# Optimization experiments

Hardware: AMD Instinct MI355X
Metric: run time of the kernel (lower is better)

## Reference

```python
import jax, jax.numpy as jnp
import numpy as np

B, S, D, H = 2, 2048, 1024, 16
HD = D // H


def setup_inputs() -> dict:
    key = jax.random.key(0)
    ks = jax.random.split(key, 12)
    s = 1.0 / np.sqrt(D)
    inp = {
        "queries": jax.random.normal(ks[0], (B, S, D), jnp.float32),
        "keys": jax.random.normal(ks[1], (B, S, D), jnp.float32),
        "values": jax.random.normal(ks[2], (B, S, D), jnp.float32),
        # True = masked out (causal upper triangle)
        "attn_mask": jnp.triu(jnp.ones((S, S), bool), k=1),
        "W_q": jax.random.normal(ks[3], (D, D), jnp.float32) * s,
        "b_q": jnp.zeros((D,), jnp.float32),
        "W_k": jax.random.normal(ks[4], (D, D), jnp.float32) * s,
        "b_k": jnp.zeros((D,), jnp.float32),
        "W_v": jax.random.normal(ks[5], (D, D), jnp.float32) * s,
        "b_v": jnp.zeros((D,), jnp.float32),
        "W_o": jax.random.normal(ks[6], (D, D), jnp.float32) * s,
        "b_o": jnp.zeros((D,), jnp.float32),
    }
    return inp


def _split_heads(x):
    b, s, _ = x.shape
    return x.reshape(b, s, H, HD).transpose(0, 2, 1, 3)  # (B,H,S,HD)


def reference(queries, keys, values, attn_mask, W_q, b_q, W_k, b_k, W_v, b_v, W_o, b_o):
    Q = _split_heads(queries @ W_q + b_q)
    K = _split_heads(keys @ W_k + b_k)
    V = _split_heads(values @ W_v + b_v)
    scale = 1.0 / np.sqrt(HD)
    scores = jnp.einsum("bhqd,bhkd->bhqk", Q, K) * scale  # (B,H,S,S)
    scores = jnp.where(attn_mask, jnp.float32(-1e9), scores)
    probs = jax.nn.softmax(scores, axis=-1)
    ctx = jnp.einsum("bhqk,bhkd->bhqd", probs, V)
    ctx = ctx.transpose(0, 2, 1, 3).reshape(queries.shape[0], queries.shape[1], D)
    return ctx @ W_o + b_o
```

## Files before the change

kernel.cpp:

```cpp
#include <hip/hip_runtime.h>
#include <hip/hip_bf16.h>
#include <math.h>

typedef __bf16 bf16x8 __attribute__((ext_vector_type(8)));
typedef float f32x4 __attribute__((ext_vector_type(4)));
typedef unsigned short u16x8 __attribute__((ext_vector_type(8)));
typedef unsigned short u16x4 __attribute__((ext_vector_type(4)));

static __device__ __forceinline__ unsigned short f2bf(float f) {
    union { float f; unsigned u; } v; v.f = f;
    unsigned r = v.u + 0x7fffu + ((v.u >> 16) & 1u);
    return (unsigned short)(r >> 16);
}

static __device__ __forceinline__ float exp2fast(float x) {
    return __builtin_exp2f(x);
}

static __device__ __forceinline__ void gload16(const void* g, void* l) {
    __builtin_amdgcn_global_load_lds((const __attribute__((address_space(1))) unsigned int*)g,
                                     (__attribute__((address_space(3))) unsigned int*)l, 16, 0, 0);
}

#define MFMA16(a, b, c) __builtin_amdgcn_mfma_f32_16x16x32_bf16((a), (b), (c), 0, 0, 0)

static __device__ __forceinline__ bf16x8 frag_swz(const unsigned short* base, int row, int chunk) {
    return *(const bf16x8*)((const char*)base + row * 128 + (((chunk ^ row) & 7) << 4));
}

__global__ void conv_bf16_kernel(const float* __restrict__ in, unsigned short* __restrict__ out) {
    const size_t i = ((size_t)blockIdx.x * 256 + threadIdx.x) * 8;
    f32x4 v0 = *(const f32x4*)(in + i);
    f32x4 v1 = *(const f32x4*)(in + i + 4);
    u16x8 o;
#pragma unroll
    for (int j = 0; j < 4; ++j) { o[j] = f2bf(v0[j]); o[j + 4] = f2bf(v1[j]); }
    *(u16x8*)(out + i) = o;
}

__global__ void conv_wt_kernel(const float* __restrict__ W, unsigned short* __restrict__ Wt) {
    __shared__ __align__(16) unsigned short Ws[64][66];
    const int t = threadIdx.x;
    const int r0 = blockIdx.y * 64;
    const int c0 = blockIdx.x * 64;
#pragma unroll
    for (int p = 0; p < 4; ++p) {
        int lin = p * 256 + t;
        int r = lin >> 4, cc = (lin & 15) * 4;
        f32x4 v = *(const f32x4*)(W + (size_t)(r0 + r) * 1024 + c0 + cc);
#pragma unroll
        for (int j = 0; j < 4; ++j) Ws[r][cc + j] = f2bf(v[j]);
    }
    __syncthreads();
#pragma unroll
    for (int p = 0; p < 2; ++p) {
        int lin = p * 256 + t;
        int n = lin >> 3, kc = (lin & 7) * 8;
        u16x8 o;
#pragma unroll
        for (int j = 0; j < 8; ++j) o[j] = Ws[kc + j][n];
        *(u16x8*)(Wt + (size_t)(c0 + n) * 1024 + r0 + kc) = o;
    }
}

template<int OMODE>
__global__ __launch_bounds__(256, 2)
void gemm_bt(const unsigned short* __restrict__ A, const unsigned short* __restrict__ Bt,
             const float* __restrict__ bias, void* __restrict__ Outp,
             int M, int N, int K, float oscale)
{
    __shared__ __align__(16) unsigned short As[2][128 * 64];
    __shared__ __align__(16) unsigned short Bs[2][128 * 64];

    const int t = threadIdx.x, lane = t & 63, w = t >> 6;
    const int lr = lane & 15, lh = lane >> 4;
    const int m0 = blockIdx.y * 128, n0 = blockIdx.x * 128;
    const int wm = (w >> 1) * 64, wn = (w & 1) * 64;
    const int nkt = K >> 6;
    const int wbase = (t & 0xC0) * 8;

    f32x4 acc[4][4];
#pragma unroll
    for (int i = 0; i < 4; ++i)
#pragma unroll
        for (int j = 0; j < 4; ++j)
#pragma unroll
            for (int e = 0; e < 4; ++e) acc[i][j][e] = 0.0f;

    auto stage = [&](int buf, int kt) {
        const int k0 = kt << 6;
#pragma unroll
        for (int q = 0; q < 4; ++q) {
            int lin = q * 256 + t;
            int row = lin >> 3, sc = (lin ^ (lin >> 3)) & 7;
            gload16(A + (size_t)(m0 + row) * K + k0 + sc * 8, &As[buf][q * 2048 + wbase]);
        }
#pragma unroll
        for (int q = 0; q < 4; ++q) {
            int lin = q * 256 + t;
            int row = lin >> 3, sc = (lin ^ (lin >> 3)) & 7;
            gload16(Bt + (size_t)(n0 + row) * K + k0 + sc * 8, &Bs[buf][q * 2048 + wbase]);
        }
    };

    stage(0, 0);
    for (int kt = 0; kt < nkt; ++kt) {
        __syncthreads();
        if (kt + 1 < nkt) stage((kt + 1) & 1, kt + 1);
        const unsigned short* as = As[kt & 1];
        const unsigned short* bs = Bs[kt & 1];
#pragma unroll
        for (int kb = 0; kb < 2; ++kb) {
            bf16x8 a[4], b[4];
#pragma unroll
            for (int i = 0; i < 4; ++i) a[i] = frag_swz(as, wm + i * 16 + lr, kb * 4 + lh);
#pragma unroll
            for (int j = 0; j < 4; ++j) b[j] = frag_swz(bs, wn + j * 16 + lr, kb * 4 + lh);
#pragma unroll
            for (int i = 0; i < 4; ++i)
#pragma unroll
                for (int j = 0; j < 4; ++j)
                    acc[i][j] = MFMA16(a[i], b[j], acc[i][j]);
        }
    }

#pragma unroll
    for (int i = 0; i < 4; ++i) {
#pragma unroll
        for (int j = 0; j < 4; ++j) {
            const int gcol = n0 + wn + j * 16 + lr;
            const float bv = bias[gcol];
            if (OMODE == 0) {
#pragma unroll
                for (int r = 0; r < 4; ++r) {
                    const int grow = m0 + wm + i * 16 + lh * 4 + r;
                    ((float*)Outp)[(size_t)grow * N + gcol] = (acc[i][j][r] + bv) * oscale;
                }
            } else if (OMODE == 1) {
#pragma unroll
                for (int r = 0; r < 4; ++r) {
                    const int grow = m0 + wm + i * 16 + lh * 4 + r;
                    const int b_ = grow >> 11, s_ = grow & 2047;
                    const int h_ = gcol >> 6, hd_ = gcol & 63;
                    ((unsigned short*)Outp)[((size_t)((b_ * 16 + h_) * 2048 + s_) << 6) + hd_] =
                        f2bf((acc[i][j][r] + bv) * oscale);
                }
            } else {
                const int grow0 = m0 + wm + i * 16 + lh * 4;
                const int b_ = grow0 >> 11, s_ = grow0 & 2047;
                const int h_ = gcol >> 6, hd_ = gcol & 63;
                u16x4 pk;
#pragma unroll
                for (int r = 0; r < 4; ++r) pk[r] = f2bf((acc[i][j][r] + bv) * oscale);
                *(u16x4*)((unsigned short*)Outp + (((size_t)((b_ * 16 + h_) * 64 + hd_)) << 11) + s_) = pk;
            }
        }
    }
}

__global__ __launch_bounds__(256, 2)
void attn_kernel(const unsigned short* __restrict__ Qp,
                 const unsigned short* __restrict__ Kp,
                 const unsigned short* __restrict__ Vtp,
                 unsigned short* __restrict__ Cp)
{
    __shared__ __align__(16) unsigned short Ks[2][64 * 64];
    __shared__ __align__(16) unsigned short Vs[2][64 * 64];
    __shared__ __align__(16) unsigned short Pl[4][16 * 64];

    const int t = threadIdx.x, lane = t & 63, w = t >> 6;
    const int lr = lane & 15, lh = lane >> 4;
    const int wbase = (t & 0xC0) * 8;

    const int g = blockIdx.x;
    const int local = g >> 3;
    const int bh = (g & 7) * 4 + (local >> 4);
    const int qA = local & 15;
    const size_t baseQK = (size_t)bh * (2048 * 64);
    const size_t baseV  = (size_t)bh * (64 * 2048);

    auto stageKV = [&](int buf, int kv0) {
#pragma unroll
        for (int q = 0; q < 2; ++q) {
            int lin = q * 256 + t;
            int row = lin >> 3, sc = (lin ^ (lin >> 3)) & 7;
            gload16(Kp + baseQK + (size_t)(kv0 + row) * 64 + sc * 8, &Ks[buf][q * 2048 + wbase]);
        }
#pragma unroll
        for (int q = 0; q < 2; ++q) {
            int lin = q * 256 + t;
            int row = lin >> 3, sc = (lin ^ (lin >> 3)) & 7;
            gload16(Vtp + baseV + (size_t)row * 2048 + kv0 + sc * 8, &Vs[buf][q * 2048 + wbase]);
        }
    };

    unsigned short* pl = &Pl[w][0];
    const int b_ = bh >> 4, h_ = bh & 15;

    for (int qi = 0; qi < 2; ++qi) {
        const int qt = qi ? (31 - qA) : qA;
        const int q0w = qt * 64 + w * 16;
        const int ntiles = qt + 1;

        const unsigned short* qrow = Qp + baseQK + (size_t)(q0w + lr) * 64 + lh * 8;
        const bf16x8 qf0 = *(const bf16x8*)qrow;
        const bf16x8 qf1 = *(const bf16x8*)(qrow + 32);

        f32x4 o[4]; float m[4], l[4];
#pragma unroll
        for (int i = 0; i < 4; ++i) {
#pragma unroll
            for (int e = 0; e < 4; ++e) o[i][e] = 0.0f;
            m[i] = -INFINITY; l[i] = 0.0f;
        }

        __syncthreads();
        stageKV(0, 0);
        for (int tt = 0; tt < ntiles; ++tt) {
            __syncthreads();
            if (tt + 1 < ntiles) stageKV((tt + 1) & 1, (tt + 1) * 64);
            const unsigned short* ks = Ks[tt & 1];
            const unsigned short* vs = Vs[tt & 1];

            f32x4 s[4];
#pragma unroll
            for (int c = 0; c < 4; ++c) {
#pragma unroll
                for (int e = 0; e < 4; ++e) s[c][e] = 0.0f;
                s[c] = MFMA16(qf0, frag_swz(ks, c * 16 + lr, lh), s[c]);
                s[c] = MFMA16(qf1, frag_swz(ks, c * 16 + lr, 4 + lh), s[c]);
            }

            const bool diag = (tt == qt);
            const int kv0 = tt * 64;
#pragma unroll
            for (int r = 0; r < 4; ++r) {
                const int row = lh * 4 + r;
                const int grow = q0w + row;
                float tv[4];
#pragma unroll
                for (int c = 0; c < 4; ++c) {
                    float x = s[c][r];
                    if (diag && (kv0 + c * 16 + lr > grow)) x = -1e30f;
                    tv[c] = x;
                }
                float cm = fmaxf(fmaxf(tv[0], tv[1]), fmaxf(tv[2], tv[3]));
                cm = fmaxf(cm, __shfl_xor(cm, 1));
                cm = fmaxf(cm, __shfl_xor(cm, 2));
                cm = fmaxf(cm, __shfl_xor(cm, 4));
                cm = fmaxf(cm, __shfl_xor(cm, 8));
                if (!__all(cm <= m[r] + 11.0f)) {
                    const float mn = fmaxf(m[r], cm);
                    const float al = exp2fast(m[r] - mn);
#pragma unroll
                    for (int hc = 0; hc < 4; ++hc) o[hc][r] *= al;
                    l[r] *= al;
                    m[r] = mn;
                }
                float rs = 0.0f;
#pragma unroll
                for (int c = 0; c < 4; ++c) {
                    const float p = exp2fast(tv[c] - m[r]);
                    rs += p;
                    *(unsigned short*)((char*)pl + row * 128 +
                        ((c * 32 + lr * 2) ^ ((row & 7) << 4))) = f2bf(p);
                }
                l[r] += rs;
            }

            const bf16x8 pf0 = frag_swz(pl, lr, lh);
            const bf16x8 pf1 = frag_swz(pl, lr, 4 + lh);
#pragma unroll
            for (int hc = 0; hc < 4; ++hc) {
                o[hc] = MFMA16(pf0, frag_swz(vs, hc * 16 + lr, lh), o[hc]);
                o[hc] = MFMA16(pf1, frag_swz(vs, hc * 16 + lr, 4 + lh), o[hc]);
            }
        }

#pragma unroll
        for (int r = 0; r < 4; ++r) {
            float sum = l[r];
            sum += __shfl_xor(sum, 1);
            sum += __shfl_xor(sum, 2);
            sum += __shfl_xor(sum, 4);
            sum += __shfl_xor(sum, 8);
            const float inv = 1.0f / sum;
            const int srow = q0w + lh * 4 + r;
#pragma unroll
            for (int hc = 0; hc < 4; ++hc) {
                Cp[(size_t)(b_ * 2048 + srow) * 1024 + h_ * 64 + hc * 16 + lr] =
                    f2bf(o[hc][r] * inv);
            }
        }
    }
}

extern "C" void kernel_launch(void* const* d_in, const int* in_sizes, int n_in,
                              void* d_out, int out_size, void* d_ws, size_t ws_size,
                              hipStream_t stream)
{
    const float* queries = (const float*)d_in[0];
    const float* keys    = (const float*)d_in[1];
    const float* values  = (const float*)d_in[2];
    const float* W_q = (const float*)d_in[4];
    const float* b_q = (const float*)d_in[5];
    const float* W_k = (const float*)d_in[6];
    const float* b_k = (const float*)d_in[7];
    const float* W_v = (const float*)d_in[8];
    const float* b_v = (const float*)d_in[9];
    const float* W_o = (const float*)d_in[10];
    const float* b_o = (const float*)d_in[11];

    constexpr size_t NE = (size_t)4 * 1024 * 1024;
    constexpr size_t WE = (size_t)1024 * 1024;
    unsigned short* qc  = (unsigned short*)d_ws;
    unsigned short* kc  = qc + NE;
    unsigned short* vc  = kc + NE;
    unsigned short* wqT = vc + NE;
    unsigned short* wkT = wqT + WE;
    unsigned short* wvT = wkT + WE;
    unsigned short* woT = wvT + WE;
    unsigned short* Qb  = woT + WE;
    unsigned short* Kb  = Qb + NE;
    unsigned short* Vtb = Kb + NE;
    unsigned short* Cb  = Vtb + NE;

    const int M = 4096, N = 1024, K = 1024;
    const float qscale = 0.125f * 1.44269504f;

    conv_bf16_kernel<<<2048, 256, 0, stream>>>(queries, qc);
    conv_bf16_kernel<<<2048, 256, 0, stream>>>(keys, kc);
    conv_bf16_kernel<<<2048, 256, 0, stream>>>(values, vc);
    conv_wt_kernel<<<dim3(16, 16), 256, 0, stream>>>(W_q, wqT);
    conv_wt_kernel<<<dim3(16, 16), 256, 0, stream>>>(W_k, wkT);
    conv_wt_kernel<<<dim3(16, 16), 256, 0, stream>>>(W_v, wvT);
    conv_wt_kernel<<<dim3(16, 16), 256, 0, stream>>>(W_o, woT);

    gemm_bt<1><<<dim3(8, 32), 256, 0, stream>>>(qc, wqT, b_q, Qb, M, N, K, qscale);
    gemm_bt<1><<<dim3(8, 32), 256, 0, stream>>>(kc, wkT, b_k, Kb, M, N, K, 1.0f);
    gemm_bt<2><<<dim3(8, 32), 256, 0, stream>>>(vc, wvT, b_v, Vtb, M, N, K, 1.0f);

    attn_kernel<<<512, 256, 0, stream>>>(Qb, Kb, Vtb, Cb);

    gemm_bt<0><<<dim3(8, 32), 256, 0, stream>>>(Cb, woT, b_o, d_out, M, N, K, 1.0f);
}
```

Measured before the change: 301.9 us.

## Batch conversion and QKV GEMM launches, retile output GEMM, trim softmax shuffles

Merges the three input conversions into one launch, the four weight transposes into one launch, and the three QKV projections into a single z-indexed GEMM launch. The QKV GEMM drops double buffering to single-buffered LDS and raises occupancy to 3 blocks/SM. The output GEMM moves to 64-row tiles so 512 blocks fill the device. In attention, the cross-lane max reduction is done only when the rescale branch fires, and the bf16 conversion uses the native cast. The main aim is cutting launch overhead and raising GPU fill. The risks are losing load/compute overlap in the QKV GEMM and a different rounding for the attention probabilities.

```diff
diff --git a/kernel.cpp b/kernel.cpp
--- a/kernel.cpp
+++ b/kernel.cpp
@@ -28,18 +28,27 @@
     return *(const bf16x8*)((const char*)base + row * 128 + (((chunk ^ row) & 7) << 4));
 }
 
-__global__ void conv_bf16_kernel(const float* __restrict__ in, unsigned short* __restrict__ out) {
-    const size_t i = ((size_t)blockIdx.x * 256 + threadIdx.x) * 8;
+struct Cv3 { const float* in[3]; unsigned short* out[3]; };
+
+__global__ void conv3_kernel(Cv3 a) {
+    const int x = blockIdx.x;
+    const int sel = x >> 11;
+    const size_t i = (((size_t)(x & 2047)) * 256 + threadIdx.x) * 8;
+    const float* in = a.in[sel];
     f32x4 v0 = *(const f32x4*)(in + i);
     f32x4 v1 = *(const f32x4*)(in + i + 4);
     u16x8 o;
 #pragma unroll
     for (int j = 0; j < 4; ++j) { o[j] = f2bf(v0[j]); o[j + 4] = f2bf(v1[j]); }
-    *(u16x8*)(out + i) = o;
-}
-
-__global__ void conv_wt_kernel(const float* __restrict__ W, unsigned short* __restrict__ Wt) {
+    *(u16x8*)(a.out[sel] + i) = o;
+}
+
+struct Cw4 { const float* W[4]; unsigned short* Wt[4]; };
+
+__global__ void conv_wt4_kernel(Cw4 a) {
     __shared__ __align__(16) unsigned short Ws[64][66];
+    const float* W = a.W[blockIdx.z];
+    unsigned short* Wt = a.Wt[blockIdx.z];
     const int t = threadIdx.x;
     const int r0 = blockIdx.y * 64;
     const int c0 = blockIdx.x * 64;
@@ -63,20 +72,31 @@
     }
 }
 
-template<int OMODE>
-__global__ __launch_bounds__(256, 2)
-void gemm_bt(const unsigned short* __restrict__ A, const unsigned short* __restrict__ Bt,
-             const float* __restrict__ bias, void* __restrict__ Outp,
-             int M, int N, int K, float oscale)
+struct QkvArgs {
+    const unsigned short* A[3];
+    const unsigned short* Wt[3];
+    const float* bias[3];
+    unsigned short* out[3];
+    float scale[3];
+};
+
+__global__ __launch_bounds__(256, 3)
+void gemm_qkv(QkvArgs p)
 {
-    __shared__ __align__(16) unsigned short As[2][128 * 64];
-    __shared__ __align__(16) unsigned short Bs[2][128 * 64];
+    __shared__ __align__(16) unsigned short As[128 * 64];
+    __shared__ __align__(16) unsigned short Bs[128 * 64];
+
+    const int z = blockIdx.z;
+    const unsigned short* A  = p.A[z];
+    const unsigned short* Bt = p.Wt[z];
+    const float* bias = p.bias[z];
+    unsigned short* out = p.out[z];
+    const float oscale = p.scale[z];
 
     const int t = threadIdx.x, lane = t & 63, w = t >> 6;
     const int lr = lane & 15, lh = lane >> 4;
     const int m0 = blockIdx.y * 128, n0 = blockIdx.x * 128;
     const int wm = (w >> 1) * 64, wn = (w & 1) * 64;
-    const int nkt = K >> 6;
     const int wbase = (t & 0xC0) * 8;
 
     f32x4 acc[4][4];
@@ -87,35 +107,29 @@
 #pragma unroll
             for (int e = 0; e < 4; ++e) acc[i][j][e] = 0.0f;
 
-    auto stage = [&](int buf, int kt) {
+    for (int kt = 0; kt < 16; ++kt) {
         const int k0 = kt << 6;
+        __syncthreads();
 #pragma unroll
         for (int q = 0; q < 4; ++q) {
             int lin = q * 256 + t;
             int row = lin >> 3, sc = (lin ^ (lin >> 3)) & 7;
-            gload16(A + (size_t)(m0 + row) * K + k0 + sc * 8, &As[buf][q * 2048 + wbase]);
+            gload16(A + (size_t)(m0 + row) * 1024 + k0 + sc * 8, &As[q * 2048 + wbase]);
         }
 #pragma unroll
         for (int q = 0; q < 4; ++q) {
             int lin = q * 256 + t;
             int row = lin >> 3, sc = (lin ^ (lin >> 3)) & 7;
-            gload16(Bt + (size_t)(n0 + row) * K + k0 + sc * 8, &Bs[buf][q * 2048 + wbase]);
-        }
-    };
-
-    stage(0, 0);
-    for (int kt = 0; kt < nkt; ++kt) {
+            gload16(Bt + (size_t)(n0 + row) * 1024 + k0 + sc * 8, &Bs[q * 2048 + wbase]);
+        }
         __syncthreads();
-        if (kt + 1 < nkt) stage((kt + 1) & 1, kt + 1);
-        const unsigned short* as = As[kt & 1];
-        const unsigned short* bs = Bs[kt & 1];
 #pragma unroll
         for (int kb = 0; kb < 2; ++kb) {
             bf16x8 a[4], b[4];
 #pragma unroll
-            for (int i = 0; i < 4; ++i) a[i] = frag_swz(as, wm + i * 16 + lr, kb * 4 + lh);
-#pragma unroll
-            for (int j = 0; j < 4; ++j) b[j] = frag_swz(bs, wn + j * 16 + lr, kb * 4 + lh);
+            for (int i = 0; i < 4; ++i) a[i] = frag_swz(As, wm + i * 16 + lr, kb * 4 + lh);
+#pragma unroll
+            for (int j = 0; j < 4; ++j) b[j] = frag_swz(Bs, wn + j * 16 + lr, kb * 4 + lh);
 #pragma unroll
             for (int i = 0; i < 4; ++i)
 #pragma unroll
@@ -130,29 +144,95 @@
         for (int j = 0; j < 4; ++j) {
             const int gcol = n0 + wn + j * 16 + lr;
             const float bv = bias[gcol];
-            if (OMODE == 0) {
-#pragma unroll
-                for (int r = 0; r < 4; ++r) {
-                    const int grow = m0 + wm + i * 16 + lh * 4 + r;
-                    ((float*)Outp)[(size_t)grow * N + gcol] = (acc[i][j][r] + bv) * oscale;
-                }
-            } else if (OMODE == 1) {
+            const int h_ = gcol >> 6, hd_ = gcol & 63;
+            if (z == 2) {
+                const int grow0 = m0 + wm + i * 16 + lh * 4;
+                const int b_ = grow0 >> 11, s_ = grow0 & 2047;
+                u16x4 pk;
+#pragma unroll
+                for (int r = 0; r < 4; ++r) pk[r] = f2bf((acc[i][j][r] + bv) * oscale);
+                *(u16x4*)(out + (((size_t)((b_ * 16 + h_) * 64 + hd_)) << 11) + s_) = pk;
+            } else {
 #pragma unroll
                 for (int r = 0; r < 4; ++r) {
                     const int grow = m0 + wm + i * 16 + lh * 4 + r;
                     const int b_ = grow >> 11, s_ = grow & 2047;
-                    const int h_ = gcol >> 6, hd_ = gcol & 63;
-                    ((unsigned short*)Outp)[((size_t)((b_ * 16 + h_) * 2048 + s_) << 6) + hd_] =
+                    out[((size_t)((b_ * 16 + h_) * 2048 + s_) << 6) + hd_] =
                         f2bf((acc[i][j][r] + bv) * oscale);
                 }
-            } else {
-                const int grow0 = m0 + wm + i * 16 + lh * 4;
-                const int b_ = grow0 >> 11, s_ = grow0 & 2047;
-                const int h_ = gcol >> 6, hd_ = gcol & 63;
-                u16x4 pk;
-#pragma unroll
-                for (int r = 0; r < 4; ++r) pk[r] = f2bf((acc[i][j][r] + bv) * oscale);
-                *(u16x4*)((unsigned short*)Outp + (((size_t)((b_ * 16 + h_) * 64 + hd_)) << 11) + s_) = pk;
+            }
+        }
+    }
+}
+
+__global__ __launch_bounds__(256, 3)
+void gemm_o(const unsigned short* __restrict__ A, const unsigned short* __restrict__ Bt,
+            const float* __restrict__ bias, float* __restrict__ Out)
+{
+    __shared__ __align__(16) unsigned short As[2][64 * 64];
+    __shared__ __align__(16) unsigned short Bs[2][128 * 64];
+
+    const int t = threadIdx.x, lane = t & 63, w = t >> 6;
+    const int lr = lane & 15, lh = lane >> 4;
+    const int m0 = blockIdx.y * 64, n0 = blockIdx.x * 128;
+    const int wm = (w >> 1) * 32, wn = (w & 1) * 64;
+    const int wbase = (t & 0xC0) * 8;
+
+    f32x4 acc[2][4];
+#pragma unroll
+    for (int i = 0; i < 2; ++i)
+#pragma unroll
+        for (int j = 0; j < 4; ++j)
+#pragma unroll
+            for (int e = 0; e < 4; ++e) acc[i][j][e] = 0.0f;
+
+    auto stage = [&](int buf, int kt) {
+        const int k0 = kt << 6;
+#pragma unroll
+        for (int q = 0; q < 2; ++q) {
+            int lin = q * 256 + t;
+            int row = lin >> 3, sc = (lin ^ (lin >> 3)) & 7;
+            gload16(A + (size_t)(m0 + row) * 1024 + k0 + sc * 8, &As[buf][q * 2048 + wbase]);
+        }
+#pragma unroll
+        for (int q = 0; q < 4; ++q) {
+            int lin = q * 256 + t;
+            int row = lin >> 3, sc = (lin ^ (lin >> 3)) & 7;
+            gload16(Bt + (size_t)(n0 + row) * 1024 + k0 + sc * 8, &Bs[buf][q * 2048 + wbase]);
+        }
+    };
+
+    stage(0, 0);
+    for (int kt = 0; kt < 16; ++kt) {
+        __syncthreads();
+        if (kt + 1 < 16) stage((kt + 1) & 1, kt + 1);
+        const unsigned short* as = As[kt & 1];
+        const unsigned short* bs = Bs[kt & 1];
+#pragma unroll
+        for (int kb = 0; kb < 2; ++kb) {
+            bf16x8 a[2], b[4];
+#pragma unroll
+            for (int i = 0; i < 2; ++i) a[i] = frag_swz(as, wm + i * 16 + lr, kb * 4 + lh);
+#pragma unroll
+            for (int j = 0; j < 4; ++j) b[j] = frag_swz(bs, wn + j * 16 + lr, kb * 4 + lh);
+#pragma unroll
+            for (int i = 0; i < 2; ++i)
+#pragma unroll
+                for (int j = 0; j < 4; ++j)
+                    acc[i][j] = MFMA16(a[i], b[j], acc[i][j]);
+        }
+    }
+
+#pragma unroll
+    for (int i = 0; i < 2; ++i) {
+#pragma unroll
+        for (int j = 0; j < 4; ++j) {
+            const int gcol = n0 + wn + j * 16 + lr;
+            const float bv = bias[gcol];
+#pragma unroll
+            for (int r = 0; r < 4; ++r) {
+                const int grow = m0 + wm + i * 16 + lh * 4 + r;
+                Out[(size_t)grow * 1024 + gcol] = acc[i][j][r] + bv;
             }
         }
     }
@@ -244,12 +324,13 @@
                     if (diag && (kv0 + c * 16 + lr > grow)) x = -1e30f;
                     tv[c] = x;
                 }
-                float cm = fmaxf(fmaxf(tv[0], tv[1]), fmaxf(tv[2], tv[3]));
-                cm = fmaxf(cm, __shfl_xor(cm, 1));
-                cm = fmaxf(cm, __shfl_xor(cm, 2));
-                cm = fmaxf(cm, __shfl_xor(cm, 4));
-                cm = fmaxf(cm, __shfl_xor(cm, 8));
-                if (!__all(cm <= m[r] + 11.0f)) {
+                const float lmax = fmaxf(fmaxf(tv[0], tv[1]), fmaxf(tv[2], tv[3]));
+                if (!__all(lmax <= m[r] + 11.0f)) {
+                    float cm = lmax;
+                    cm = fmaxf(cm, __shfl_xor(cm, 1));
+                    cm = fmaxf(cm, __shfl_xor(cm, 2));
+                    cm = fmaxf(cm, __shfl_xor(cm, 4));
+                    cm = fmaxf(cm, __shfl_xor(cm, 8));
                     const float mn = fmaxf(m[r], cm);
                     const float al = exp2fast(m[r] - mn);
 #pragma unroll
@@ -260,10 +341,10 @@
                 float rs = 0.0f;
 #pragma unroll
                 for (int c = 0; c < 4; ++c) {
-                    const float p = exp2fast(tv[c] - m[r]);
-                    rs += p;
-                    *(unsigned short*)((char*)pl + row * 128 +
-                        ((c * 32 + lr * 2) ^ ((row & 7) << 4))) = f2bf(p);
+                    const float pv = exp2fast(tv[c] - m[r]);
+                    rs += pv;
+                    *(__bf16*)((char*)pl + row * 128 +
+                        ((c * 32 + lr * 2) ^ ((row & 7) << 4))) = (__bf16)pv;
                 }
                 l[r] += rs;
             }
@@ -325,22 +406,25 @@
     unsigned short* Vtb = Kb + NE;
     unsigned short* Cb  = Vtb + NE;
 
-    const int M = 4096, N = 1024, K = 1024;
     const float qscale = 0.125f * 1.44269504f;
 
-    conv_bf16_kernel<<<2048, 256, 0, stream>>>(queries, qc);
-    conv_bf16_kernel<<<2048, 256, 0, stream>>>(keys, kc);
-    conv_bf16_kernel<<<2048, 256, 0, stream>>>(values, vc);
-    conv_wt_kernel<<<dim3(16, 16), 256, 0, stream>>>(W_q, wqT);
-    conv_wt_kernel<<<dim3(16, 16), 256, 0, stream>>>(W_k, wkT);
-    conv_wt_kernel<<<dim3(16, 16), 256, 0, stream>>>(W_v, wvT);
-    conv_wt_kernel<<<dim3(16, 16), 256, 0, stream>>>(W_o, woT);
-
-    gemm_bt<1><<<dim3(8, 32), 256, 0, stream>>>(qc, wqT, b_q, Qb, M, N, K, qscale);
-    gemm_bt<1><<<dim3(8, 32), 256, 0, stream>>>(kc, wkT, b_k, Kb, M, N, K, 1.0f);
-    gemm_bt<2><<<dim3(8, 32), 256, 0, stream>>>(vc, wvT, b_v, Vtb, M, N, K, 1.0f);
+    Cv3 cv;
+    cv.in[0] = queries; cv.in[1] = keys; cv.in[2] = values;
+    cv.out[0] = qc; cv.out[1] = kc; cv.out[2] = vc;
+    conv3_kernel<<<6144, 256, 0, stream>>>(cv);
+
+    Cw4 cw;
+    cw.W[0] = W_q; cw.W[1] = W_k; cw.W[2] = W_v; cw.W[3] = W_o;
+    cw.Wt[0] = wqT; cw.Wt[1] = wkT; cw.Wt[2] = wvT; cw.Wt[3] = woT;
+    conv_wt4_kernel<<<dim3(16, 16, 4), 256, 0, stream>>>(cw);
+
+    QkvArgs qp;
+    qp.A[0] = qc;  qp.Wt[0] = wqT; qp.bias[0] = b_q; qp.out[0] = Qb;  qp.scale[0] = qscale;
+    qp.A[1] = kc;  qp.Wt[1] = wkT; qp.bias[1] = b_k; qp.out[1] = Kb;  qp.scale[1] = 1.0f;
+    qp.A[2] = vc;  qp.Wt[2] = wvT; qp.bias[2] = b_v; qp.out[2] = Vtb; qp.scale[2] = 1.0f;
+    gemm_qkv<<<dim3(8, 32, 3), 256, 0, stream>>>(qp);
 
     attn_kernel<<<512, 256, 0, stream>>>(Qb, Kb, Vtb, Cb);
 
-    gemm_bt<0><<<dim3(8, 32), 256, 0, stream>>>(Cb, woT, b_o, d_out, M, N, K, 1.0f);
-}
+    gemm_o<<<dim3(8, 64), 256, 0, stream>>>(Cb, woT, b_o, (float*)d_out);
+}
```

Measured after the change: 245.5 us. -18.7%, faster.
